# Kernel optimization log

Measured on AMD Instinct MI355X. Metric: run time of the kernel, lower is better.

## Reference

```python
import jax, jax.numpy as jnp
import numpy as np

N = 50000
E = 800000
IN_C = 128
HID = 64
HEADS = 4
OUT_C = 64
NEG_SLOPE = 0.2


def gat_conv(x, edge_index, W, att_src, att_dst, bias, heads, out_ch, concat):
    """PyG-style GATConv (add_self_loops=True, eval mode: no dropout)."""
    n = x.shape[0]
    loop = jnp.arange(n, dtype=edge_index.dtype)
    src = jnp.concatenate([edge_index[0], loop])
    dst = jnp.concatenate([edge_index[1], loop])
    h = (x @ W).reshape(n, heads, out_ch)              # [N,H,C]
    a_s = jnp.einsum('nhc,hc->nh', h, att_src)          # [N,H]
    a_d = jnp.einsum('nhc,hc->nh', h, att_dst)
    e = jax.nn.leaky_relu(a_s[src] + a_d[dst], NEG_SLOPE)  # [E',H]
    m = jax.ops.segment_max(e, dst, num_segments=n)
    m = jnp.where(jnp.isfinite(m), m, 0.0)
    ex = jnp.exp(e - m[dst])
    denom = jax.ops.segment_sum(ex, dst, num_segments=n)
    alpha = ex / (denom[dst] + 1e-16)                   # segment softmax over incoming edges
    out = jax.ops.segment_sum(alpha[:, :, None] * h[src], dst, num_segments=n)  # [N,H,C]
    out = out.reshape(n, heads * out_ch) if concat else out.mean(axis=1)
    return out + bias


def setup_inputs() -> dict:
    key = jax.random.key(0)
    ks = jax.random.split(key, 20)
    s = 0.1
    inp = {
        'x': jax.random.normal(ks[0], (N, IN_C), dtype=jnp.float32),
        'pos_edge_index': jax.random.randint(ks[1], (2, E), 0, N, dtype=jnp.int32),
        'neg_edge_index': jax.random.randint(ks[2], (2, E), 0, N, dtype=jnp.int32),
        # layer 0 pos
        'W0p': jax.random.normal(ks[3], (IN_C, HEADS * HID), jnp.float32) * s,
        'asrc0p': jax.random.normal(ks[4], (HEADS, HID), jnp.float32) * s,
        'adst0p': jax.random.normal(ks[5], (HEADS, HID), jnp.float32) * s,
        'b0p': jnp.zeros((HEADS * HID,), jnp.float32),
        # layer 0 neg
        'W0n': jax.random.normal(ks[6], (IN_C, HEADS * HID), jnp.float32) * s,
        'asrc0n': jax.random.normal(ks[7], (HEADS, HID), jnp.float32) * s,
        'adst0n': jax.random.normal(ks[8], (HEADS, HID), jnp.float32) * s,
        'b0n': jnp.zeros((HEADS * HID,), jnp.float32),
        # layer 1 pos (heads=1, concat=False)
        'W1p': jax.random.normal(ks[9], (HEADS * HID, OUT_C), jnp.float32) * s,
        'asrc1p': jax.random.normal(ks[10], (1, OUT_C), jnp.float32) * s,
        'adst1p': jax.random.normal(ks[11], (1, OUT_C), jnp.float32) * s,
        'b1p': jnp.zeros((OUT_C,), jnp.float32),
        # layer 1 neg
        'W1n': jax.random.normal(ks[12], (HEADS * HID, OUT_C), jnp.float32) * s,
        'asrc1n': jax.random.normal(ks[13], (1, OUT_C), jnp.float32) * s,
        'adst1n': jax.random.normal(ks[14], (1, OUT_C), jnp.float32) * s,
        'b1n': jnp.zeros((OUT_C,), jnp.float32),
    }
    return inp


def reference(x, pos_edge_index, neg_edge_index,
              W0p, asrc0p, adst0p, b0p,
              W0n, asrc0n, adst0n, b0n,
              W1p, asrc1p, adst1p, b1p,
              W1n, asrc1n, adst1n, b1n):
    xp = gat_conv(x, pos_edge_index, W0p, asrc0p, adst0p, b0p, HEADS, HID, True)
    xn = gat_conv(x, neg_edge_index, W0n, asrc0n, adst0n, b0n, HEADS, HID, True)
    h = jax.nn.elu(xp - xn)  # dropout is identity in eval mode
    op = gat_conv(h, pos_edge_index, W1p, asrc1p, adst1p, b1p, 1, OUT_C, False)
    on = gat_conv(h, neg_edge_index, W1n, asrc1n, adst1n, b1n, 1, OUT_C, False)
    return op - on
```

## Files before the change

kernel.cpp:

```cpp
#include <hip/hip_runtime.h>
#include <cstdint>

#define N_NODES 50000
#define N_EDGES 800000

typedef __attribute__((ext_vector_type(8))) short bf16x8;
typedef __attribute__((ext_vector_type(4))) float f32x4;

__device__ __forceinline__ float lrelu(float x) { return x >= 0.f ? x : 0.2f * x; }

__device__ __forceinline__ unsigned short f2b(float f) {
  unsigned int u = __float_as_uint(f);
  u += 0x7FFFu + ((u >> 16) & 1u);
  return (unsigned short)(u >> 16);
}
__device__ __forceinline__ float blo(unsigned int u) { return __uint_as_float(u << 16); }
__device__ __forceinline__ float bhi(unsigned int u) { return __uint_as_float(u & 0xFFFF0000u); }


__global__ __launch_bounds__(256) void k_hist2(const int* __restrict__ ep, const int* __restrict__ en,
                                               int* __restrict__ cntP, int* __restrict__ cntN, int E, int half) {
  int b = blockIdx.x;
  const int* ei = (b < half) ? ep : en;
  int* cnt = (b < half) ? cntP : cntN;
  int e = (b % half) * 256 + threadIdx.x;
  if (e < E) atomicAdd(&cnt[ei[E + e]], 1);
}

__global__ __launch_bounds__(256) void k_scan_partial2(const int* __restrict__ cntP, const int* __restrict__ cntN,
                                                       int* __restrict__ partP, int* __restrict__ partN,
                                                       int N, int half) {
  int b = blockIdx.x;
  const int* cnt = (b < half) ? cntP : cntN;
  int* partial = (b < half) ? partP : partN;
  int bb = b % half;
  int t = threadIdx.x;
  int sum = 0;
#pragma unroll
  for (int i = 0; i < 4; i++) {
    int idx = bb * 1024 + i * 256 + t;
    if (idx < N) sum += cnt[idx];
  }
#pragma unroll
  for (int o = 32; o; o >>= 1) sum += __shfl_xor(sum, o);
  __shared__ int sh[4];
  if ((t & 63) == 0) sh[t >> 6] = sum;
  __syncthreads();
  if (t == 0) partial[bb] = sh[0] + sh[1] + sh[2] + sh[3];
}

__global__ __launch_bounds__(64) void k_scan_top2(const int* __restrict__ partP, const int* __restrict__ partN,
                                                  int* __restrict__ prefP, int* __restrict__ prefN,
                                                  int nb, int* __restrict__ offPN, int* __restrict__ offNN, int total) {
  const int* partial = (blockIdx.x == 0) ? partP : partN;
  int* pref = (blockIdx.x == 0) ? prefP : prefN;
  int* offN = (blockIdx.x == 0) ? offPN : offNN;
  int l = threadIdx.x;
  int v = (l < nb) ? partial[l] : 0;
  int x = v;
#pragma unroll
  for (int o = 1; o < 64; o <<= 1) {
    int y = __shfl_up(x, o);
    if (l >= o) x += y;
  }
  if (l < nb) pref[l] = x - v;
  if (l == 0) *offN = total;
}

__global__ __launch_bounds__(256) void k_scan_final2(const int* __restrict__ cntP, const int* __restrict__ cntN,
                                                     const int* __restrict__ prefP, const int* __restrict__ prefN,
                                                     int* __restrict__ offP, int* __restrict__ offN,
                                                     int N, int half) {
  int b = blockIdx.x;
  const int* cnt = (b < half) ? cntP : cntN;
  const int* pref = (b < half) ? prefP : prefN;
  int* off = (b < half) ? offP : offN;
  int bb = b % half;
  int t = threadIdx.x;
  int idx0 = bb * 1024 + t * 4;
  int v0 = (idx0 + 0 < N) ? cnt[idx0 + 0] : 0;
  int v1 = (idx0 + 1 < N) ? cnt[idx0 + 1] : 0;
  int v2 = (idx0 + 2 < N) ? cnt[idx0 + 2] : 0;
  int v3 = (idx0 + 3 < N) ? cnt[idx0 + 3] : 0;
  int s = v0 + v1 + v2 + v3;
  int lane = t & 63, w = t >> 6;
  int x = s;
#pragma unroll
  for (int o = 1; o < 64; o <<= 1) {
    int y = __shfl_up(x, o);
    if (lane >= o) x += y;
  }
  __shared__ int wtot[4];
  if (lane == 63) wtot[w] = x;
  __syncthreads();
  int woff = 0;
#pragma unroll
  for (int i = 0; i < 4; i++)
    if (i < w) woff += wtot[i];
  int excl = pref[bb] + woff + (x - s);
  if (idx0 + 0 < N) off[idx0 + 0] = excl;
  excl += v0;
  if (idx0 + 1 < N) off[idx0 + 1] = excl;
  excl += v1;
  if (idx0 + 2 < N) off[idx0 + 2] = excl;
  excl += v2;
  if (idx0 + 3 < N) off[idx0 + 3] = excl;
}

__global__ __launch_bounds__(256) void k_scatter2(const int* __restrict__ ep, const int* __restrict__ en,
                                                  const int* __restrict__ offP, const int* __restrict__ offN,
                                                  int* __restrict__ cntP, int* __restrict__ cntN,
                                                  int* __restrict__ srtP, int* __restrict__ srtN, int E, int half) {
  int b = blockIdx.x;
  const int* ei = (b < half) ? ep : en;
  const int* off = (b < half) ? offP : offN;
  int* cnt = (b < half) ? cntP : cntN;
  int* srt = (b < half) ? srtP : srtN;
  int e = (b % half) * 256 + threadIdx.x;
  if (e < E) {
    int s = ei[e], d = ei[E + e];
    int p = atomicSub(&cnt[d], 1) - 1;
    srt[off[d] + p] = s;
  }
}


__global__ __launch_bounds__(256) void k_prep(const float* __restrict__ x,
                                              const float* __restrict__ W0p, const float* __restrict__ W0n,
                                              const float* __restrict__ W1p, const float* __restrict__ W1n,
                                              unsigned short* __restrict__ xb,
                                              unsigned short* __restrict__ w0f,
                                              unsigned short* __restrict__ w1f) {
  int b = blockIdx.x, t = threadIdx.x;
  if (b < 3125) {
    int base = (b * 256 + t) * 8;
    float4 v0 = *(const float4*)&x[base];
    float4 v1 = *(const float4*)&x[base + 4];
    ushort4 a, c;
    a.x = f2b(v0.x); a.y = f2b(v0.y); a.z = f2b(v0.z); a.w = f2b(v0.w);
    c.x = f2b(v1.x); c.y = f2b(v1.y); c.z = f2b(v1.z); c.w = f2b(v1.w);
    *(ushort4*)&xb[base] = a;
    *(ushort4*)&xb[base + 4] = c;
  } else if (b < 3157) {
    int tid = (b - 3125) * 256 + t;
    int lane = tid & 63;
    int rest = tid >> 6;
    int ks = rest & 3; rest >>= 2;
    int n = rest & 3;
    int g = rest >> 2;
    int col = (g & 3) * 64 + n * 16 + (lane & 15);
    const float* W = (g < 4) ? W0p : W0n;
    size_t dst = ((((size_t)(g * 4 + n)) * 4 + ks) * 64 + lane) * 8;
#pragma unroll
    for (int j = 0; j < 8; j++) {
      int k = ks * 32 + (lane >> 4) * 8 + j;
      w0f[dst + j] = f2b(W[k * 256 + col]);
    }
  } else {
    int tid = (b - 3157) * 256 + t;
    int lane = tid & 63;
    int rest = tid >> 6;
    int ks = rest & 7; rest >>= 3;
    int n = rest & 3;
    int g = rest >> 2;
    int col = n * 16 + (lane & 15);
    const float* W = g ? W1n : W1p;
    size_t dst = ((((size_t)(g * 4 + n)) * 8 + ks) * 64 + lane) * 8;
#pragma unroll
    for (int j = 0; j < 8; j++) {
      int k = ks * 32 + (lane >> 4) * 8 + j;
      w1f[dst + j] = f2b(W[k * 64 + col]);
    }
  }
}


template <int KSTEPS, int CBF16, int H, int NC>
__global__ __launch_bounds__(256) void k_mgemm(const unsigned short* __restrict__ Ab,
                                               const unsigned short* __restrict__ Bf,
                                               unsigned short* __restrict__ Cb, float* __restrict__ Cf,
                                               int Nrows,
                                               const float* __restrict__ attSP, const float* __restrict__ attDP,
                                               const float* __restrict__ attSN, const float* __restrict__ attDN,
                                               float* __restrict__ oSP, float* __restrict__ oDP,
                                               float* __restrict__ oSN, float* __restrict__ oDN) {
  constexpr int K = KSTEPS * 32;
  int wm = threadIdx.x >> 6, lane = threadIdx.x & 63;
  int row0 = blockIdx.x * 128 + wm * 32;
  int g = blockIdx.y;
  const bf16x8* Bv = (const bf16x8*)Bf;
  const bf16x8* Av = (const bf16x8*)Ab;

  f32x4 acc[2][4];
#pragma unroll
  for (int mi = 0; mi < 2; mi++)
#pragma unroll
    for (int n = 0; n < 4; n++) acc[mi][n] = (f32x4){0.f, 0.f, 0.f, 0.f};

  int r0 = row0 + (lane & 15);
  int r1 = r0 + 16;
  bool v0 = r0 < Nrows, v1 = r1 < Nrows;
  size_t arow0 = (size_t)r0 * (K / 8) + (lane >> 4);
  size_t arow1 = (size_t)r1 * (K / 8) + (lane >> 4);
  const bf16x8 az = {0, 0, 0, 0, 0, 0, 0, 0};

  for (int kh = 0; kh < KSTEPS / 4; kh++) {
#pragma unroll
    for (int k4 = 0; k4 < 4; k4++) {
      int ks = kh * 4 + k4;
      bf16x8 a0 = v0 ? Av[arow0 + ks * 4] : az;
      bf16x8 a1 = v1 ? Av[arow1 + ks * 4] : az;
      bf16x8 b0 = Bv[((size_t)(g * 4 + 0) * KSTEPS + ks) * 64 + lane];
      bf16x8 b1 = Bv[((size_t)(g * 4 + 1) * KSTEPS + ks) * 64 + lane];
      bf16x8 b2 = Bv[((size_t)(g * 4 + 2) * KSTEPS + ks) * 64 + lane];
      bf16x8 b3 = Bv[((size_t)(g * 4 + 3) * KSTEPS + ks) * 64 + lane];
      acc[0][0] = __builtin_amdgcn_mfma_f32_16x16x32_bf16(a0, b0, acc[0][0], 0, 0, 0);
      acc[0][1] = __builtin_amdgcn_mfma_f32_16x16x32_bf16(a0, b1, acc[0][1], 0, 0, 0);
      acc[0][2] = __builtin_amdgcn_mfma_f32_16x16x32_bf16(a0, b2, acc[0][2], 0, 0, 0);
      acc[0][3] = __builtin_amdgcn_mfma_f32_16x16x32_bf16(a0, b3, acc[0][3], 0, 0, 0);
      acc[1][0] = __builtin_amdgcn_mfma_f32_16x16x32_bf16(a1, b0, acc[1][0], 0, 0, 0);
      acc[1][1] = __builtin_amdgcn_mfma_f32_16x16x32_bf16(a1, b1, acc[1][1], 0, 0, 0);
      acc[1][2] = __builtin_amdgcn_mfma_f32_16x16x32_bf16(a1, b2, acc[1][2], 0, 0, 0);
      acc[1][3] = __builtin_amdgcn_mfma_f32_16x16x32_bf16(a1, b3, acc[1][3], 0, 0, 0);
    }
  }

#pragma unroll
  for (int mi = 0; mi < 2; mi++)
#pragma unroll
    for (int n = 0; n < 4; n++)
#pragma unroll
      for (int reg = 0; reg < 4; reg++) {
        int row = row0 + mi * 16 + (lane >> 4) * 4 + reg;
        int col = g * 64 + n * 16 + (lane & 15);
        if (row < Nrows) {
          if (CBF16)
            Cb[(size_t)row * NC + col] = f2b(acc[mi][n][reg]);
          else
            Cf[(size_t)row * NC + col] = acc[mi][n][reg];
        }
      }

  constexpr int POSG = NC / 128;
  int isNeg = (g >= POSG) ? 1 : 0;
  int head = isNeg ? g - POSG : g;
  const float* wS = (isNeg ? attSN : attSP) + head * 64;
  const float* wD = (isNeg ? attDN : attDP) + head * 64;
  float* oS = isNeg ? oSN : oSP;
  float* oD = isNeg ? oDN : oDP;
  float ws0 = wS[0 * 16 + (lane & 15)], ws1 = wS[1 * 16 + (lane & 15)];
  float ws2 = wS[2 * 16 + (lane & 15)], ws3 = wS[3 * 16 + (lane & 15)];
  float wd0 = wD[0 * 16 + (lane & 15)], wd1 = wD[1 * 16 + (lane & 15)];
  float wd2 = wD[2 * 16 + (lane & 15)], wd3 = wD[3 * 16 + (lane & 15)];
#pragma unroll
  for (int mi = 0; mi < 2; mi++)
#pragma unroll
    for (int reg = 0; reg < 4; reg++) {
      float ps = acc[mi][0][reg] * ws0 + acc[mi][1][reg] * ws1 + acc[mi][2][reg] * ws2 + acc[mi][3][reg] * ws3;
      float pd = acc[mi][0][reg] * wd0 + acc[mi][1][reg] * wd1 + acc[mi][2][reg] * wd2 + acc[mi][3][reg] * wd3;
#pragma unroll
      for (int o = 1; o < 16; o <<= 1) {
        ps += __shfl_xor(ps, o);
        pd += __shfl_xor(pd, o);
      }
      int row = row0 + mi * 16 + (lane >> 4) * 4 + reg;
      if ((lane & 15) == 0 && row < Nrows) {
        oS[(size_t)row * H + head] = ps;
        oD[(size_t)row * H + head] = pd;
      }
    }
}


__global__ __launch_bounds__(256) void k_sa0(const float* __restrict__ asP, const float* __restrict__ adP,
                                             const int* __restrict__ offP, const int* __restrict__ srtP,
                                             float* __restrict__ alphaP, float* __restrict__ invP,
                                             float* __restrict__ wslfP,
                                             const float* __restrict__ asN, const float* __restrict__ adN,
                                             const int* __restrict__ offN, const int* __restrict__ srtN,
                                             float* __restrict__ alphaN, float* __restrict__ invN,
                                             float* __restrict__ wslfN, int N) {
  int n = blockIdx.x * 4 + (threadIdx.x >> 6);
  if (n >= N) return;
  int l = threadIdx.x & 63;
  {
    int base = offP[n], deg = offP[n + 1] - base;
    float4 ad4 = *(const float4*)&adP[(size_t)n * 4];
    float s0 = 0.f, s1 = 0.f, s2 = 0.f, s3 = 0.f;
    for (int i = l; i < deg; i += 64) {
      int s = srtP[base + i];
      float4 av = *(const float4*)&asP[(size_t)s * 4];
      float4 ex;
      ex.x = __expf(lrelu(av.x + ad4.x));
      ex.y = __expf(lrelu(av.y + ad4.y));
      ex.z = __expf(lrelu(av.z + ad4.z));
      ex.w = __expf(lrelu(av.w + ad4.w));
      *(float4*)&alphaP[(size_t)(base + i) * 4] = ex;
      s0 += ex.x; s1 += ex.y; s2 += ex.z; s3 += ex.w;
    }
#pragma unroll
    for (int o = 32; o; o >>= 1) {
      s0 += __shfl_xor(s0, o);
      s1 += __shfl_xor(s1, o);
      s2 += __shfl_xor(s2, o);
      s3 += __shfl_xor(s3, o);
    }
    if (l == 0) {
      float4 as4 = *(const float4*)&asP[(size_t)n * 4];
      float e0 = __expf(lrelu(as4.x + ad4.x));
      float e1 = __expf(lrelu(as4.y + ad4.y));
      float e2 = __expf(lrelu(as4.z + ad4.z));
      float e3 = __expf(lrelu(as4.w + ad4.w));
      float i0 = 1.f / (s0 + e0 + 1e-16f);
      float i1 = 1.f / (s1 + e1 + 1e-16f);
      float i2 = 1.f / (s2 + e2 + 1e-16f);
      float i3 = 1.f / (s3 + e3 + 1e-16f);
      *(float4*)&invP[(size_t)n * 4] = make_float4(i0, i1, i2, i3);
      *(float4*)&wslfP[(size_t)n * 4] = make_float4(e0 * i0, e1 * i1, e2 * i2, e3 * i3);
    }
  }
  {
    int base = offN[n], deg = offN[n + 1] - base;
    float4 ad4 = *(const float4*)&adN[(size_t)n * 4];
    float s0 = 0.f, s1 = 0.f, s2 = 0.f, s3 = 0.f;
    for (int i = l; i < deg; i += 64) {
      int s = srtN[base + i];
      float4 av = *(const float4*)&asN[(size_t)s * 4];
      float4 ex;
      ex.x = __expf(lrelu(av.x + ad4.x));
      ex.y = __expf(lrelu(av.y + ad4.y));
      ex.z = __expf(lrelu(av.z + ad4.z));
      ex.w = __expf(lrelu(av.w + ad4.w));
      *(float4*)&alphaN[(size_t)(base + i) * 4] = ex;
      s0 += ex.x; s1 += ex.y; s2 += ex.z; s3 += ex.w;
    }
#pragma unroll
    for (int o = 32; o; o >>= 1) {
      s0 += __shfl_xor(s0, o);
      s1 += __shfl_xor(s1, o);
      s2 += __shfl_xor(s2, o);
      s3 += __shfl_xor(s3, o);
    }
    if (l == 0) {
      float4 as4 = *(const float4*)&asN[(size_t)n * 4];
      float e0 = __expf(lrelu(as4.x + ad4.x));
      float e1 = __expf(lrelu(as4.y + ad4.y));
      float e2 = __expf(lrelu(as4.z + ad4.z));
      float e3 = __expf(lrelu(as4.w + ad4.w));
      float i0 = 1.f / (s0 + e0 + 1e-16f);
      float i1 = 1.f / (s1 + e1 + 1e-16f);
      float i2 = 1.f / (s2 + e2 + 1e-16f);
      float i3 = 1.f / (s3 + e3 + 1e-16f);
      *(float4*)&invN[(size_t)n * 4] = make_float4(i0, i1, i2, i3);
      *(float4*)&wslfN[(size_t)n * 4] = make_float4(e0 * i0, e1 * i1, e2 * i2, e3 * i3);
    }
  }
}


__device__ __forceinline__ float4 gather0b(const unsigned short* __restrict__ h0b, int colElem,
                                           const float* __restrict__ alpha, int hl,
                                           const int* __restrict__ srt, int base, int deg) {
  float4 acc = make_float4(0.f, 0.f, 0.f, 0.f);
  for (int j = 0; j < deg; j += 8) {
    int idx[8];
    float w[8];
#pragma unroll
    for (int s2 = 0; s2 < 8; s2++) {
      int jj = j + s2;
      bool v = jj < deg;
      int p = base + (v ? jj : 0);
      idx[s2] = srt[p];
      w[s2] = v ? alpha[(size_t)p * 4 + hl] : 0.f;
    }
#pragma unroll
    for (int s2 = 0; s2 < 8; s2++) {
      uint2 hv = *(const uint2*)&h0b[(size_t)idx[s2] * 512 + colElem];
      acc.x = fmaf(w[s2], blo(hv.x), acc.x);
      acc.y = fmaf(w[s2], bhi(hv.x), acc.y);
      acc.z = fmaf(w[s2], blo(hv.y), acc.z);
      acc.w = fmaf(w[s2], bhi(hv.y), acc.w);
    }
  }
  return acc;
}

__global__ __launch_bounds__(256) void k_gather0(const unsigned short* __restrict__ h0b,
                                                 const int* __restrict__ offP, const int* __restrict__ srtP,
                                                 const float* __restrict__ alphaP, const float* __restrict__ invP,
                                                 const float* __restrict__ wslfP,
                                                 const int* __restrict__ offN, const int* __restrict__ srtN,
                                                 const float* __restrict__ alphaN, const float* __restrict__ invN,
                                                 const float* __restrict__ wslfN,
                                                 const float* __restrict__ bP, const float* __restrict__ bN,
                                                 unsigned short* __restrict__ xb, int N) {
  int n = blockIdx.x * 4 + (threadIdx.x >> 6);
  if (n >= N) return;
  int l = threadIdx.x & 63;
  int hl = l >> 4;

  int baseP = offP[n], degP = offP[n + 1] - baseP;
  float4 accP = gather0b(h0b, l * 4, alphaP, hl, srtP, baseP, degP);
  {
    float iv = invP[(size_t)n * 4 + hl];
    float ws = wslfP[(size_t)n * 4 + hl];
    uint2 hs = *(const uint2*)&h0b[(size_t)n * 512 + l * 4];
    accP.x = fmaf(accP.x, iv, ws * blo(hs.x));
    accP.y = fmaf(accP.y, iv, ws * bhi(hs.x));
    accP.z = fmaf(accP.z, iv, ws * blo(hs.y));
    accP.w = fmaf(accP.w, iv, ws * bhi(hs.y));
  }

  int baseN = offN[n], degN = offN[n + 1] - baseN;
  float4 accN = gather0b(h0b, 256 + l * 4, alphaN, hl, srtN, baseN, degN);
  {
    float iv = invN[(size_t)n * 4 + hl];
    float ws = wslfN[(size_t)n * 4 + hl];
    uint2 hs = *(const uint2*)&h0b[(size_t)n * 512 + 256 + l * 4];
    accN.x = fmaf(accN.x, iv, ws * blo(hs.x));
    accN.y = fmaf(accN.y, iv, ws * bhi(hs.x));
    accN.z = fmaf(accN.z, iv, ws * blo(hs.y));
    accN.w = fmaf(accN.w, iv, ws * bhi(hs.y));
  }

  float4 bp = *(const float4*)&bP[l * 4];
  float4 bn = *(const float4*)&bN[l * 4];
  float rx = accP.x + bp.x - accN.x - bn.x;
  float ry = accP.y + bp.y - accN.y - bn.y;
  float rz = accP.z + bp.z - accN.z - bn.z;
  float rw = accP.w + bp.w - accN.w - bn.w;
  rx = rx > 0.f ? rx : expm1f(rx);
  ry = ry > 0.f ? ry : expm1f(ry);
  rz = rz > 0.f ? rz : expm1f(rz);
  rw = rw > 0.f ? rw : expm1f(rw);
  ushort4 r;
  r.x = f2b(rx); r.y = f2b(ry); r.z = f2b(rz); r.w = f2b(rw);
  *(ushort4*)&xb[(size_t)n * 256 + l * 4] = r;
}


__global__ __launch_bounds__(256) void k_sa1(const float* __restrict__ asP, const float* __restrict__ adP,
                                             const int* __restrict__ offP, const int* __restrict__ srtP,
                                             float* __restrict__ alphaP, float* __restrict__ invP,
                                             float* __restrict__ wslfP,
                                             const float* __restrict__ asN, const float* __restrict__ adN,
                                             const int* __restrict__ offN, const int* __restrict__ srtN,
                                             float* __restrict__ alphaN, float* __restrict__ invN,
                                             float* __restrict__ wslfN, int N) {
  int n = blockIdx.x * 4 + (threadIdx.x >> 6);
  if (n >= N) return;
  int l = threadIdx.x & 63;
  {
    int base = offP[n], deg = offP[n + 1] - base;
    float ad = adP[n];
    float s = 0.f;
    for (int i = l; i < deg; i += 64) {
      float ex = __expf(lrelu(asP[srtP[base + i]] + ad));
      alphaP[base + i] = ex;
      s += ex;
    }
#pragma unroll
    for (int o = 32; o; o >>= 1) s += __shfl_xor(s, o);
    if (l == 0) {
      float se = __expf(lrelu(asP[n] + ad));
      float iv = 1.f / (s + se + 1e-16f);
      invP[n] = iv;
      wslfP[n] = se * iv;
    }
  }
  {
    int base = offN[n], deg = offN[n + 1] - base;
    float ad = adN[n];
    float s = 0.f;
    for (int i = l; i < deg; i += 64) {
      float ex = __expf(lrelu(asN[srtN[base + i]] + ad));
      alphaN[base + i] = ex;
      s += ex;
    }
#pragma unroll
    for (int o = 32; o; o >>= 1) s += __shfl_xor(s, o);
    if (l == 0) {
      float se = __expf(lrelu(asN[n] + ad));
      float iv = 1.f / (s + se + 1e-16f);
      invN[n] = iv;
      wslfN[n] = se * iv;
    }
  }
}

__device__ __forceinline__ float gather1b(const float* __restrict__ h1, int colIdx,
                                          const float* __restrict__ alpha,
                                          const int* __restrict__ srt, int base, int deg) {
  float acc = 0.f;
  for (int j = 0; j < deg; j += 8) {
    int idx[8];
    float w[8];
#pragma unroll
    for (int s2 = 0; s2 < 8; s2++) {
      int jj = j + s2;
      bool v = jj < deg;
      int p = base + (v ? jj : 0);
      idx[s2] = srt[p];
      w[s2] = v ? alpha[p] : 0.f;
    }
#pragma unroll
    for (int s2 = 0; s2 < 8; s2++) acc = fmaf(w[s2], h1[(size_t)idx[s2] * 128 + colIdx], acc);
  }
  return acc;
}

__global__ __launch_bounds__(256) void k_gather1(const float* __restrict__ h1,
                                                 const int* __restrict__ offP, const int* __restrict__ srtP,
                                                 const float* __restrict__ alphaP, const float* __restrict__ invP,
                                                 const float* __restrict__ wslfP,
                                                 const int* __restrict__ offN, const int* __restrict__ srtN,
                                                 const float* __restrict__ alphaN, const float* __restrict__ invN,
                                                 const float* __restrict__ wslfN,
                                                 const float* __restrict__ bP, const float* __restrict__ bN,
                                                 float* __restrict__ out, int N) {
  int n = blockIdx.x * 4 + (threadIdx.x >> 6);
  if (n >= N) return;
  int l = threadIdx.x & 63;

  int baseP = offP[n], degP = offP[n + 1] - baseP;
  float accP = gather1b(h1, l, alphaP, srtP, baseP, degP);
  accP = fmaf(accP, invP[n], wslfP[n] * h1[(size_t)n * 128 + l]);

  int baseN = offN[n], degN = offN[n + 1] - baseN;
  float accN = gather1b(h1, 64 + l, alphaN, srtN, baseN, degN);
  accN = fmaf(accN, invN[n], wslfN[n] * h1[(size_t)n * 128 + 64 + l]);

  out[(size_t)n * 64 + l] = (accP + bP[l]) - (accN + bN[l]);
}


extern "C" void kernel_launch(void* const* d_in, const int* in_sizes, int n_in,
                              void* d_out, int out_size, void* d_ws, size_t ws_size,
                              hipStream_t stream) {
  const float* x = (const float*)d_in[0];
  const int* ep = (const int*)d_in[1];
  const int* en = (const int*)d_in[2];
  const float* W0p = (const float*)d_in[3];
  const float* asrc0p = (const float*)d_in[4];
  const float* adst0p = (const float*)d_in[5];
  const float* b0p = (const float*)d_in[6];
  const float* W0n = (const float*)d_in[7];
  const float* asrc0n = (const float*)d_in[8];
  const float* adst0n = (const float*)d_in[9];
  const float* b0n = (const float*)d_in[10];
  const float* W1p = (const float*)d_in[11];
  const float* asrc1p = (const float*)d_in[12];
  const float* adst1p = (const float*)d_in[13];
  const float* b1p = (const float*)d_in[14];
  const float* W1n = (const float*)d_in[15];
  const float* asrc1n = (const float*)d_in[16];
  const float* adst1n = (const float*)d_in[17];
  const float* b1n = (const float*)d_in[18];

  const int N = N_NODES, E = N_EDGES;
  char* base = (char*)d_ws;
  size_t o = 0;
  auto alloc = [&](size_t bytes) -> void* {
    void* r = base + o;
    o = (o + bytes + 255) & ~(size_t)255;
    return r;
  };
  int* cnt_p = (int*)alloc((size_t)N * 4);
  int* cnt_n = (int*)alloc((size_t)N * 4);
  size_t cntBytes = o;
  int* off_p = (int*)alloc((size_t)(N + 1) * 4);
  int* off_n = (int*)alloc((size_t)(N + 1) * 4);
  int* part_p = (int*)alloc(1024 * 4);
  int* part_n = (int*)alloc(1024 * 4);
  int* pref_p = (int*)alloc(1024 * 4);
  int* pref_n = (int*)alloc(1024 * 4);
  int* srt_p = (int*)alloc((size_t)E * 4);
  int* srt_n = (int*)alloc((size_t)E * 4);
  unsigned short* xb16 = (unsigned short*)alloc((size_t)N * 128 * 2);
  unsigned short* w0f = (unsigned short*)alloc(65536 * 2);
  unsigned short* w1f = (unsigned short*)alloc(32768 * 2);
  unsigned short* h0b = (unsigned short*)alloc((size_t)N * 512 * 2);
  float* as0p = (float*)alloc((size_t)N * 4 * 4);
  float* ad0p = (float*)alloc((size_t)N * 4 * 4);
  float* as0n = (float*)alloc((size_t)N * 4 * 4);
  float* ad0n = (float*)alloc((size_t)N * 4 * 4);
  float* as1p = (float*)alloc((size_t)N * 4);
  float* ad1p = (float*)alloc((size_t)N * 4);
  float* as1n = (float*)alloc((size_t)N * 4);
  float* ad1n = (float*)alloc((size_t)N * 4);
  float* inv0p = (float*)alloc((size_t)N * 4 * 4);
  float* wslf0p = (float*)alloc((size_t)N * 4 * 4);
  float* inv0n = (float*)alloc((size_t)N * 4 * 4);
  float* wslf0n = (float*)alloc((size_t)N * 4 * 4);
  float* inv1p = (float*)alloc((size_t)N * 4);
  float* wslf1p = (float*)alloc((size_t)N * 4);
  float* inv1n = (float*)alloc((size_t)N * 4);
  float* wslf1n = (float*)alloc((size_t)N * 4);
  float* alpha0p = (float*)alloc((size_t)E * 4 * 4);
  float* alpha0n = (float*)alloc((size_t)E * 4 * 4);
  float* alpha1p = (float*)alloc((size_t)E * 4);
  float* alpha1n = (float*)alloc((size_t)E * 4);
  unsigned short* xbufb = (unsigned short*)alloc((size_t)N * 256 * 2);
  float* h1 = (float*)alloc((size_t)N * 128 * 4);

  hipMemsetAsync(base, 0, cntBytes, stream);

  int egrid = (E + 255) / 256;
  int nb = (N + 1023) / 1024;
  k_hist2<<<2 * egrid, 256, 0, stream>>>(ep, en, cnt_p, cnt_n, E, egrid);
  k_scan_partial2<<<2 * nb, 256, 0, stream>>>(cnt_p, cnt_n, part_p, part_n, N, nb);
  k_scan_top2<<<2, 64, 0, stream>>>(part_p, part_n, pref_p, pref_n, nb, off_p + N, off_n + N, E);
  k_scan_final2<<<2 * nb, 256, 0, stream>>>(cnt_p, cnt_n, pref_p, pref_n, off_p, off_n, N, nb);
  k_scatter2<<<2 * egrid, 256, 0, stream>>>(ep, en, off_p, off_n, cnt_p, cnt_n, srt_p, srt_n, E, egrid);

  k_prep<<<3173, 256, 0, stream>>>(x, W0p, W0n, W1p, W1n, xb16, w0f, w1f);

  int ngrid = (N + 3) / 4;
  int mgrid = (N + 127) / 128;

  dim3 g0(mgrid, 8);
  k_mgemm<4, 1, 4, 512><<<g0, 256, 0, stream>>>(xb16, w0f, h0b, (float*)nullptr, N,
                                                asrc0p, adst0p, asrc0n, adst0n,
                                                as0p, ad0p, as0n, ad0n);
  k_sa0<<<ngrid, 256, 0, stream>>>(as0p, ad0p, off_p, srt_p, alpha0p, inv0p, wslf0p,
                                   as0n, ad0n, off_n, srt_n, alpha0n, inv0n, wslf0n, N);
  k_gather0<<<ngrid, 256, 0, stream>>>(h0b, off_p, srt_p, alpha0p, inv0p, wslf0p,
                                       off_n, srt_n, alpha0n, inv0n, wslf0n, b0p, b0n, xbufb, N);

  dim3 g1(mgrid, 2);
  k_mgemm<8, 0, 1, 128><<<g1, 256, 0, stream>>>(xbufb, w1f, (unsigned short*)nullptr, h1, N,
                                                asrc1p, adst1p, asrc1n, adst1n,
                                                as1p, ad1p, as1n, ad1n);
  k_sa1<<<ngrid, 256, 0, stream>>>(as1p, ad1p, off_p, srt_p, alpha1p, inv1p, wslf1p,
                                   as1n, ad1n, off_n, srt_n, alpha1n, inv1n, wslf1n, N);
  k_gather1<<<ngrid, 256, 0, stream>>>(h1, off_p, srt_p, alpha1p, inv1p, wslf1p,
                                       off_n, srt_n, alpha1n, inv1n, wslf1n, b1p, b1n, (float*)d_out, N);
}
```

Measured before the change: 577.7 us.

## Interleave pos/neg gathers and remap GEMM waves to share A rows across column groups

The gather kernels now walk the positive and negative neighbor lists in one loop instead of two sequential passes, so twice as many independent index and feature loads are in flight per iteration. The GEMM kernel gains WROWS/WCOLS template parameters, and its waves in a block now split across column groups (g) rather than only row groups. Waves that share a block therefore read the same A rows, which improves cache reuse and shrinks the grid. The cost is padding work when the two degrees differ, since the loop runs to the larger degree with masked loads, plus higher register pressure.

```diff
diff --git a/kernel.cpp b/kernel.cpp
--- a/kernel.cpp
+++ b/kernel.cpp
@@ -175,7 +175,7 @@
 }
 
 
-template <int KSTEPS, int CBF16, int H, int NC>
+template <int KSTEPS, int CBF16, int H, int NC, int WROWS, int WCOLS>
 __global__ __launch_bounds__(256) void k_mgemm(const unsigned short* __restrict__ Ab,
                                                const unsigned short* __restrict__ Bf,
                                                unsigned short* __restrict__ Cb, float* __restrict__ Cf,
@@ -185,9 +185,10 @@
                                                float* __restrict__ oSP, float* __restrict__ oDP,
                                                float* __restrict__ oSN, float* __restrict__ oDN) {
   constexpr int K = KSTEPS * 32;
-  int wm = threadIdx.x >> 6, lane = threadIdx.x & 63;
-  int row0 = blockIdx.x * 128 + wm * 32;
-  int g = blockIdx.y;
+  int w = threadIdx.x >> 6, lane = threadIdx.x & 63;
+  int wr = w / WCOLS, wc = w % WCOLS;
+  int row0 = blockIdx.x * (WROWS * 32) + wr * 32;
+  int g = blockIdx.y * WCOLS + wc;
   const bf16x8* Bv = (const bf16x8*)Bf;
   const bf16x8* Av = (const bf16x8*)Ab;
 
@@ -358,33 +359,6 @@
 }
 
 
-__device__ __forceinline__ float4 gather0b(const unsigned short* __restrict__ h0b, int colElem,
-                                           const float* __restrict__ alpha, int hl,
-                                           const int* __restrict__ srt, int base, int deg) {
-  float4 acc = make_float4(0.f, 0.f, 0.f, 0.f);
-  for (int j = 0; j < deg; j += 8) {
-    int idx[8];
-    float w[8];
-#pragma unroll
-    for (int s2 = 0; s2 < 8; s2++) {
-      int jj = j + s2;
-      bool v = jj < deg;
-      int p = base + (v ? jj : 0);
-      idx[s2] = srt[p];
-      w[s2] = v ? alpha[(size_t)p * 4 + hl] : 0.f;
-    }
-#pragma unroll
-    for (int s2 = 0; s2 < 8; s2++) {
-      uint2 hv = *(const uint2*)&h0b[(size_t)idx[s2] * 512 + colElem];
-      acc.x = fmaf(w[s2], blo(hv.x), acc.x);
-      acc.y = fmaf(w[s2], bhi(hv.x), acc.y);
-      acc.z = fmaf(w[s2], blo(hv.y), acc.z);
-      acc.w = fmaf(w[s2], bhi(hv.y), acc.w);
-    }
-  }
-  return acc;
-}
-
 __global__ __launch_bounds__(256) void k_gather0(const unsigned short* __restrict__ h0b,
                                                  const int* __restrict__ offP, const int* __restrict__ srtP,
                                                  const float* __restrict__ alphaP, const float* __restrict__ invP,
@@ -398,25 +372,55 @@
   if (n >= N) return;
   int l = threadIdx.x & 63;
   int hl = l >> 4;
+  int colP = l * 4, colN = 256 + l * 4;
 
   int baseP = offP[n], degP = offP[n + 1] - baseP;
-  float4 accP = gather0b(h0b, l * 4, alphaP, hl, srtP, baseP, degP);
+  int baseN = offN[n], degN = offN[n + 1] - baseN;
+  float4 accP = make_float4(0.f, 0.f, 0.f, 0.f);
+  float4 accN = make_float4(0.f, 0.f, 0.f, 0.f);
+  int dmax = degP > degN ? degP : degN;
+  for (int j = 0; j < dmax; j += 8) {
+    int iP[8], iN[8];
+    float wP[8], wN[8];
+#pragma unroll
+    for (int s = 0; s < 8; s++) {
+      int jj = j + s;
+      bool vP = jj < degP;
+      int pP = vP ? baseP + jj : 0;
+      iP[s] = srtP[pP];
+      wP[s] = vP ? alphaP[(size_t)pP * 4 + hl] : 0.f;
+      bool vN = jj < degN;
+      int pN = vN ? baseN + jj : 0;
+      iN[s] = srtN[pN];
+      wN[s] = vN ? alphaN[(size_t)pN * 4 + hl] : 0.f;
+    }
+#pragma unroll
+    for (int s = 0; s < 8; s++) {
+      uint2 hvP = *(const uint2*)&h0b[(size_t)iP[s] * 512 + colP];
+      uint2 hvN = *(const uint2*)&h0b[(size_t)iN[s] * 512 + colN];
+      accP.x = fmaf(wP[s], blo(hvP.x), accP.x);
+      accP.y = fmaf(wP[s], bhi(hvP.x), accP.y);
+      accP.z = fmaf(wP[s], blo(hvP.y), accP.z);
+      accP.w = fmaf(wP[s], bhi(hvP.y), accP.w);
+      accN.x = fmaf(wN[s], blo(hvN.x), accN.x);
+      accN.y = fmaf(wN[s], bhi(hvN.x), accN.y);
+      accN.z = fmaf(wN[s], blo(hvN.y), accN.z);
+      accN.w = fmaf(wN[s], bhi(hvN.y), accN.w);
+    }
+  }
   {
     float iv = invP[(size_t)n * 4 + hl];
     float ws = wslfP[(size_t)n * 4 + hl];
-    uint2 hs = *(const uint2*)&h0b[(size_t)n * 512 + l * 4];
+    uint2 hs = *(const uint2*)&h0b[(size_t)n * 512 + colP];
     accP.x = fmaf(accP.x, iv, ws * blo(hs.x));
     accP.y = fmaf(accP.y, iv, ws * bhi(hs.x));
     accP.z = fmaf(accP.z, iv, ws * blo(hs.y));
     accP.w = fmaf(accP.w, iv, ws * bhi(hs.y));
   }
-
-  int baseN = offN[n], degN = offN[n + 1] - baseN;
-  float4 accN = gather0b(h0b, 256 + l * 4, alphaN, hl, srtN, baseN, degN);
   {
     float iv = invN[(size_t)n * 4 + hl];
     float ws = wslfN[(size_t)n * 4 + hl];
-    uint2 hs = *(const uint2*)&h0b[(size_t)n * 512 + 256 + l * 4];
+    uint2 hs = *(const uint2*)&h0b[(size_t)n * 512 + colN];
     accN.x = fmaf(accN.x, iv, ws * blo(hs.x));
     accN.y = fmaf(accN.y, iv, ws * bhi(hs.x));
     accN.z = fmaf(accN.z, iv, ws * blo(hs.y));
@@ -488,27 +492,6 @@
   }
 }
 
-__device__ __forceinline__ float gather1b(const float* __restrict__ h1, int colIdx,
-                                          const float* __restrict__ alpha,
-                                          const int* __restrict__ srt, int base, int deg) {
-  float acc = 0.f;
-  for (int j = 0; j < deg; j += 8) {
-    int idx[8];
-    float w[8];
-#pragma unroll
-    for (int s2 = 0; s2 < 8; s2++) {
-      int jj = j + s2;
-      bool v = jj < deg;
-      int p = base + (v ? jj : 0);
-      idx[s2] = srt[p];
-      w[s2] = v ? alpha[p] : 0.f;
-    }
-#pragma unroll
-    for (int s2 = 0; s2 < 8; s2++) acc = fmaf(w[s2], h1[(size_t)idx[s2] * 128 + colIdx], acc);
-  }
-  return acc;
-}
-
 __global__ __launch_bounds__(256) void k_gather1(const float* __restrict__ h1,
                                                  const int* __restrict__ offP, const int* __restrict__ srtP,
                                                  const float* __restrict__ alphaP, const float* __restrict__ invP,
@@ -523,11 +506,31 @@
   int l = threadIdx.x & 63;
 
   int baseP = offP[n], degP = offP[n + 1] - baseP;
-  float accP = gather1b(h1, l, alphaP, srtP, baseP, degP);
+  int baseN = offN[n], degN = offN[n + 1] - baseN;
+  float accP = 0.f, accN = 0.f;
+  int dmax = degP > degN ? degP : degN;
+  for (int j = 0; j < dmax; j += 8) {
+    int iP[8], iN[8];
+    float wP[8], wN[8];
+#pragma unroll
+    for (int s = 0; s < 8; s++) {
+      int jj = j + s;
+      bool vP = jj < degP;
+      int pP = vP ? baseP + jj : 0;
+      iP[s] = srtP[pP];
+      wP[s] = vP ? alphaP[pP] : 0.f;
+      bool vN = jj < degN;
+      int pN = vN ? baseN + jj : 0;
+      iN[s] = srtN[pN];
+      wN[s] = vN ? alphaN[pN] : 0.f;
+    }
+#pragma unroll
+    for (int s = 0; s < 8; s++) {
+      accP = fmaf(wP[s], h1[(size_t)iP[s] * 128 + l], accP);
+      accN = fmaf(wN[s], h1[(size_t)iN[s] * 128 + 64 + l], accN);
+    }
+  }
   accP = fmaf(accP, invP[n], wslfP[n] * h1[(size_t)n * 128 + l]);
-
-  int baseN = offN[n], degN = offN[n + 1] - baseN;
-  float accN = gather1b(h1, 64 + l, alphaN, srtN, baseN, degN);
   accN = fmaf(accN, invN[n], wslfN[n] * h1[(size_t)n * 128 + 64 + l]);
 
   out[(size_t)n * 64 + l] = (accP + bP[l]) - (accN + bN[l]);
@@ -616,21 +619,20 @@
   k_prep<<<3173, 256, 0, stream>>>(x, W0p, W0n, W1p, W1n, xb16, w0f, w1f);
 
   int ngrid = (N + 3) / 4;
-  int mgrid = (N + 127) / 128;
-
-  dim3 g0(mgrid, 8);
-  k_mgemm<4, 1, 4, 512><<<g0, 256, 0, stream>>>(xb16, w0f, h0b, (float*)nullptr, N,
-                                                asrc0p, adst0p, asrc0n, adst0n,
-                                                as0p, ad0p, as0n, ad0n);
+
+  dim3 g0((N + 31) / 32, 2);
+  k_mgemm<4, 1, 4, 512, 1, 4><<<g0, 256, 0, stream>>>(xb16, w0f, h0b, (float*)nullptr, N,
+                                                      asrc0p, adst0p, asrc0n, adst0n,
+                                                      as0p, ad0p, as0n, ad0n);
   k_sa0<<<ngrid, 256, 0, stream>>>(as0p, ad0p, off_p, srt_p, alpha0p, inv0p, wslf0p,
                                    as0n, ad0n, off_n, srt_n, alpha0n, inv0n, wslf0n, N);
   k_gather0<<<ngrid, 256, 0, stream>>>(h0b, off_p, srt_p, alpha0p, inv0p, wslf0p,
                                        off_n, srt_n, alpha0n, inv0n, wslf0n, b0p, b0n, xbufb, N);
 
-  dim3 g1(mgrid, 2);
-  k_mgemm<8, 0, 1, 128><<<g1, 256, 0, stream>>>(xbufb, w1f, (unsigned short*)nullptr, h1, N,
-                                                asrc1p, adst1p, asrc1n, adst1n,
-                                                as1p, ad1p, as1n, ad1n);
+  dim3 g1((N + 63) / 64, 1);
+  k_mgemm<8, 0, 1, 128, 2, 2><<<g1, 256, 0, stream>>>(xbufb, w1f, (unsigned short*)nullptr, h1, N,
+                                                      asrc1p, adst1p, asrc1n, adst1n,
+                                                      as1p, ad1p, as1n, ad1n);
   k_sa1<<<ngrid, 256, 0, stream>>>(as1p, ad1p, off_p, srt_p, alpha1p, inv1p, wslf1p,
                                    as1n, ad1n, off_n, srt_n, alpha1n, inv1n, wslf1n, N);
   k_gather1<<<ngrid, 256, 0, stream>>>(h1, off_p, srt_p, alpha1p, inv1p, wslf1p,
```

After: 575.2 us. Within noise of the previous version (-0.4%).

## Store layer-1 features in bf16, split gather lanes across graphs, retile GEMM waves

Applied to the files above, without the earlier changes.

The layer-1 GEMM now writes h1 as bf16 instead of fp32, which halves the bytes fetched by the random per-edge gathers in the final kernel. That gather now handles the positive and negative graphs in parallel, one half-wave each with two columns per lane, and combines them with a shuffle. The GEMM template gains a wave row/column layout so several column groups run in one block, giving smaller row tiles and more blocks. Storing h1 in bf16 lowers precision. The half-wave split leaves lanes idle when the two graphs' node degrees differ.

```diff
diff --git a/kernel.cpp b/kernel.cpp
--- a/kernel.cpp
+++ b/kernel.cpp
@@ -175,7 +175,7 @@
 }
 
 
-template <int KSTEPS, int CBF16, int H, int NC>
+template <int KSTEPS, int CBF16, int H, int NC, int WROWS, int WCOLS>
 __global__ __launch_bounds__(256) void k_mgemm(const unsigned short* __restrict__ Ab,
                                                const unsigned short* __restrict__ Bf,
                                                unsigned short* __restrict__ Cb, float* __restrict__ Cf,
@@ -185,9 +185,10 @@
                                                float* __restrict__ oSP, float* __restrict__ oDP,
                                                float* __restrict__ oSN, float* __restrict__ oDN) {
   constexpr int K = KSTEPS * 32;
-  int wm = threadIdx.x >> 6, lane = threadIdx.x & 63;
-  int row0 = blockIdx.x * 128 + wm * 32;
-  int g = blockIdx.y;
+  int w = threadIdx.x >> 6, lane = threadIdx.x & 63;
+  int wr = w / WCOLS, wc = w % WCOLS;
+  int row0 = blockIdx.x * (WROWS * 32) + wr * 32;
+  int g = blockIdx.y * WCOLS + wc;
   const bf16x8* Bv = (const bf16x8*)Bf;
   const bf16x8* Av = (const bf16x8*)Ab;
 
@@ -369,7 +370,7 @@
     for (int s2 = 0; s2 < 8; s2++) {
       int jj = j + s2;
       bool v = jj < deg;
-      int p = base + (v ? jj : 0);
+      int p = v ? base + jj : 0;
       idx[s2] = srt[p];
       w[s2] = v ? alpha[(size_t)p * 4 + hl] : 0.f;
     }
@@ -488,28 +489,7 @@
   }
 }
 
-__device__ __forceinline__ float gather1b(const float* __restrict__ h1, int colIdx,
-                                          const float* __restrict__ alpha,
-                                          const int* __restrict__ srt, int base, int deg) {
-  float acc = 0.f;
-  for (int j = 0; j < deg; j += 8) {
-    int idx[8];
-    float w[8];
-#pragma unroll
-    for (int s2 = 0; s2 < 8; s2++) {
-      int jj = j + s2;
-      bool v = jj < deg;
-      int p = base + (v ? jj : 0);
-      idx[s2] = srt[p];
-      w[s2] = v ? alpha[p] : 0.f;
-    }
-#pragma unroll
-    for (int s2 = 0; s2 < 8; s2++) acc = fmaf(w[s2], h1[(size_t)idx[s2] * 128 + colIdx], acc);
-  }
-  return acc;
-}
-
-__global__ __launch_bounds__(256) void k_gather1(const float* __restrict__ h1,
+__global__ __launch_bounds__(256) void k_gather1(const unsigned short* __restrict__ h1b,
                                                  const int* __restrict__ offP, const int* __restrict__ srtP,
                                                  const float* __restrict__ alphaP, const float* __restrict__ invP,
                                                  const float* __restrict__ wslfP,
@@ -521,16 +501,50 @@
   int n = blockIdx.x * 4 + (threadIdx.x >> 6);
   if (n >= N) return;
   int l = threadIdx.x & 63;
-
-  int baseP = offP[n], degP = offP[n + 1] - baseP;
-  float accP = gather1b(h1, l, alphaP, srtP, baseP, degP);
-  accP = fmaf(accP, invP[n], wslfP[n] * h1[(size_t)n * 128 + l]);
-
-  int baseN = offN[n], degN = offN[n + 1] - baseN;
-  float accN = gather1b(h1, 64 + l, alphaN, srtN, baseN, degN);
-  accN = fmaf(accN, invN[n], wslfN[n] * h1[(size_t)n * 128 + 64 + l]);
-
-  out[(size_t)n * 64 + l] = (accP + bP[l]) - (accN + bN[l]);
+  int half = l >> 5;
+  int lh = l & 31;
+  const int* off = half ? offN : offP;
+  const int* srt = half ? srtN : srtP;
+  const float* alpha = half ? alphaN : alphaP;
+  const float* inv = half ? invN : invP;
+  const float* wslf = half ? wslfN : wslfP;
+  int base = off[n], deg = off[n + 1] - base;
+  int colB = half * 64 + lh * 2;
+
+  float ax = 0.f, ay = 0.f;
+  for (int j = 0; j < deg; j += 8) {
+    int idx[8];
+    float w[8];
+#pragma unroll
+    for (int s = 0; s < 8; s++) {
+      int jj = j + s;
+      bool v = jj < deg;
+      int p = v ? base + jj : 0;
+      idx[s] = srt[p];
+      w[s] = v ? alpha[p] : 0.f;
+    }
+#pragma unroll
+    for (int s = 0; s < 8; s++) {
+      unsigned int hv = *(const unsigned int*)&h1b[(size_t)idx[s] * 128 + colB];
+      ax = fmaf(w[s], blo(hv), ax);
+      ay = fmaf(w[s], bhi(hv), ay);
+    }
+  }
+  {
+    float iv = inv[n], ws = wslf[n];
+    unsigned int hs = *(const unsigned int*)&h1b[(size_t)n * 128 + colB];
+    ax = fmaf(ax, iv, ws * blo(hs));
+    ay = fmaf(ay, iv, ws * bhi(hs));
+  }
+  float nx = __shfl(ax, l + 32);
+  float ny = __shfl(ay, l + 32);
+  if (l < 32) {
+    int c = lh * 2;
+    float2 r;
+    r.x = (ax + bP[c]) - (nx + bN[c]);
+    r.y = (ay + bP[c + 1]) - (ny + bN[c + 1]);
+    *(float2*)&out[(size_t)n * 64 + c] = r;
+  }
 }
 
 
@@ -601,7 +615,7 @@
   float* alpha1p = (float*)alloc((size_t)E * 4);
   float* alpha1n = (float*)alloc((size_t)E * 4);
   unsigned short* xbufb = (unsigned short*)alloc((size_t)N * 256 * 2);
-  float* h1 = (float*)alloc((size_t)N * 128 * 4);
+  unsigned short* h1b = (unsigned short*)alloc((size_t)N * 128 * 2);
 
   hipMemsetAsync(base, 0, cntBytes, stream);
 
@@ -616,23 +630,22 @@
   k_prep<<<3173, 256, 0, stream>>>(x, W0p, W0n, W1p, W1n, xb16, w0f, w1f);
 
   int ngrid = (N + 3) / 4;
-  int mgrid = (N + 127) / 128;
-
-  dim3 g0(mgrid, 8);
-  k_mgemm<4, 1, 4, 512><<<g0, 256, 0, stream>>>(xb16, w0f, h0b, (float*)nullptr, N,
-                                                asrc0p, adst0p, asrc0n, adst0n,
-                                                as0p, ad0p, as0n, ad0n);
+
+  dim3 g0((N + 31) / 32, 2);
+  k_mgemm<4, 1, 4, 512, 1, 4><<<g0, 256, 0, stream>>>(xb16, w0f, h0b, (float*)nullptr, N,
+                                                      asrc0p, adst0p, asrc0n, adst0n,
+                                                      as0p, ad0p, as0n, ad0n);
   k_sa0<<<ngrid, 256, 0, stream>>>(as0p, ad0p, off_p, srt_p, alpha0p, inv0p, wslf0p,
                                    as0n, ad0n, off_n, srt_n, alpha0n, inv0n, wslf0n, N);
   k_gather0<<<ngrid, 256, 0, stream>>>(h0b, off_p, srt_p, alpha0p, inv0p, wslf0p,
                                        off_n, srt_n, alpha0n, inv0n, wslf0n, b0p, b0n, xbufb, N);
 
-  dim3 g1(mgrid, 2);
-  k_mgemm<8, 0, 1, 128><<<g1, 256, 0, stream>>>(xbufb, w1f, (unsigned short*)nullptr, h1, N,
-                                                asrc1p, adst1p, asrc1n, adst1n,
-                                                as1p, ad1p, as1n, ad1n);
+  dim3 g1((N + 63) / 64, 1);
+  k_mgemm<8, 1, 1, 128, 2, 2><<<g1, 256, 0, stream>>>(xbufb, w1f, h1b, (float*)nullptr, N,
+                                                      asrc1p, adst1p, asrc1n, adst1n,
+                                                      as1p, ad1p, as1n, ad1n);
   k_sa1<<<ngrid, 256, 0, stream>>>(as1p, ad1p, off_p, srt_p, alpha1p, inv1p, wslf1p,
                                    as1n, ad1n, off_n, srt_n, alpha1n, inv1n, wslf1n, N);
-  k_gather1<<<ngrid, 256, 0, stream>>>(h1, off_p, srt_p, alpha1p, inv1p, wslf1p,
+  k_gather1<<<ngrid, 256, 0, stream>>>(h1b, off_p, srt_p, alpha1p, inv1p, wslf1p,
                                        off_n, srt_n, alpha1n, inv1n, wslf1n, b1p, b1n, (float*)d_out, N);
 }
```

Measured after the change: 544.0 us. -5.8%, faster.
